# Performance work log

Hardware: AMD Instinct MI355X
Metric: run time of the kernel (lower is better)

The kernel has to match this reference:

```python
import jax, jax.numpy as jnp
import numpy as np

NEG = -1.0e4  # finite stand-in for log(0) of the zero initial state (exp(NEG)==0 in fp32)


def log_g(x):
    # log of g(x) = where(x>=0, x+0.5, sigmoid(x))
    return jnp.where(x >= 0, jnp.log(jax.nn.relu(x) + 0.5), -jax.nn.softplus(-x))


def setup_inputs() -> dict:
    key = jax.random.key(0)
    k1, k2, k3 = jax.random.split(key, 3)
    B, S, D, H, O = 8, 8192, 512, 512, 512
    x = jax.random.normal(k1, (B, S, D), dtype=jnp.float32)
    is_init = jnp.zeros((B,), dtype=bool)  # unused in training mode (h_0 is None)
    W_hg = jax.random.normal(k2, (2 * H, D), dtype=jnp.float32) / np.float32(np.sqrt(D))
    W_out = jax.random.normal(k3, (O, H), dtype=jnp.float32) / np.float32(np.sqrt(H))
    return {"x": x, "is_init": is_init, "W_hg": W_hg, "W_out": W_out}


def reference(x, is_init, W_hg, W_out):
    B, S, _ = x.shape
    H = W_hg.shape[0] // 2
    hg = jnp.einsum('bsd,ed->bse', x, W_hg)          # [B,S,2H]
    hidden, gate = hg[..., :H], hg[..., H:]
    log_coeffs = -jax.nn.softplus(gate)              # log(1 - z)
    log_values = -jax.nn.softplus(-gate) + log_g(hidden)  # log z + log g(h~)
    # prepend h_0 = 0 -> log(h_0) ~ NEG; pad coeffs with a leading 0
    log_values = jnp.concatenate(
        [jnp.full((B, 1, H), NEG, dtype=x.dtype), log_values], axis=1)
    log_coeffs = jnp.pad(log_coeffs, ((0, 0), (1, 0), (0, 0)))
    # Heinsen log-space associative scan
    a_star = jnp.cumsum(log_coeffs, axis=1)
    log_h = a_star + jax.lax.cumlogsumexp(log_values - a_star, axis=1)
    h = jnp.exp(log_h)[:, 1:]                        # drop the h_0 slot -> [B,S,H]
    h_n = h[:, -1:]                                  # [B,1,H]
    out = jnp.einsum('bsh,oh->bso', h, W_out)        # [B,S,O]
    return (out, h_n)
```

## Files before the change

kernel.cpp:

```cpp
#include <hip/hip_runtime.h>
#include <stdint.h>

typedef __bf16 bf16;
typedef bf16 bf16x8 __attribute__((ext_vector_type(8)));
typedef bf16 bf16x4 __attribute__((ext_vector_type(4)));
typedef float f32x4 __attribute__((ext_vector_type(4)));

#define MFMA16(a, b, c) __builtin_amdgcn_mfma_f32_16x16x32_bf16(a, b, c, 0, 0, 0)

__device__ __forceinline__ void gll16(const void* g, void* l) {
    __builtin_amdgcn_global_load_lds(
        (const __attribute__((address_space(1))) void*)g,
        (__attribute__((address_space(3))) void*)l, 16, 0, 0);
}

__device__ __forceinline__ float frcp(float x) { return __builtin_amdgcn_rcpf(x); }

__device__ __forceinline__ float bflo(uint32_t u) {
    union { uint32_t i; float f; } x; x.i = u << 16; return x.f;
}
__device__ __forceinline__ float bfhi(uint32_t u) {
    union { uint32_t i; float f; } x; x.i = u & 0xffff0000u; return x.f;
}
__device__ __forceinline__ uint32_t packcv(float c, float v) {
    union { bf16 b[2]; uint32_t u; } p;
    p.b[0] = (bf16)c; p.b[1] = (bf16)v; return p.u;
}

__global__ __launch_bounds__(256) void conv_kernel(
    const float* __restrict__ X, const float* __restrict__ Whg,
    const float* __restrict__ Wout, bf16* __restrict__ Xbf,
    bf16* __restrict__ Whg_bf, bf16* __restrict__ Wout_bf) {
    int i = blockIdx.x * 256 + threadIdx.x;
    if (i < 8388608) {
        f32x4 v = ((const f32x4*)X)[i];
        ((bf16x4*)Xbf)[i] = __builtin_convertvector(v, bf16x4);
    } else if (i < 8388608 + 131072) {
        int j = i - 8388608;
        f32x4 v = ((const f32x4*)Whg)[j];
        ((bf16x4*)Whg_bf)[j] = __builtin_convertvector(v, bf16x4);
    } else {
        int j = i - (8388608 + 131072);
        f32x4 v = ((const f32x4*)Wout)[j];
        ((bf16x4*)Wout_bf)[j] = __builtin_convertvector(v, bf16x4);
    }
}

__global__ __launch_bounds__(512, 2) void gemm1_kernel(
    const bf16* __restrict__ Xbf, const bf16* __restrict__ W,
    uint32_t* __restrict__ CV) {
    constexpr int K = 512;
    __shared__ bf16 As[2][256 * 64];
    __shared__ bf16 Bh[2][128 * 64];
    __shared__ bf16 Bg[2][128 * 64];

    const int t = threadIdx.x;
    const size_t m0 = (size_t)blockIdx.x * 256;
    const int n0 = blockIdx.y * 128;
    const int w = t >> 6, lane = t & 63;
    const int wm = (w >> 1) * 64, wn = (w & 1) * 64;
    const int r16 = lane & 15, quad = lane >> 4;
    const int sw = r16 & 7;

    f32x4 ah[4][4] = {};
    f32x4 ag[4][4] = {};

    auto stA = [&](int buf, int k0, int rbase) {
        #pragma unroll
        for (int r = rbase; r < rbase + 2; ++r) {
            int g = r * 512 + t; int row = g >> 3; int c8 = (g & 7) ^ (row & 7);
            gll16(Xbf + (m0 + row) * K + k0 + c8 * 8, &As[buf][g * 8]);
        }
    };
    auto stBh = [&](int buf, int k0) {
        #pragma unroll
        for (int r = 0; r < 2; ++r) {
            int g = r * 512 + t; int row = g >> 3; int c8 = (g & 7) ^ (row & 7);
            gll16(W + (size_t)(n0 + row) * K + k0 + c8 * 8, &Bh[buf][g * 8]);
        }
    };
    auto stBg = [&](int buf, int k0) {
        #pragma unroll
        for (int r = 0; r < 2; ++r) {
            int g = r * 512 + t; int row = g >> 3; int c8 = (g & 7) ^ (row & 7);
            gll16(W + (size_t)(512 + n0 + row) * K + k0 + c8 * 8, &Bg[buf][g * 8]);
        }
    };
    auto rdA = [&](bf16x8* d, int buf, int kg) {
        #pragma unroll
        for (int i = 0; i < 4; ++i)
            d[i] = *(const bf16x8*)&As[buf][(wm + i * 16 + r16) * 64 + (kg ^ sw) * 8];
    };
    auto rdBh = [&](bf16x8* d, int buf, int kg) {
        #pragma unroll
        for (int i = 0; i < 4; ++i)
            d[i] = *(const bf16x8*)&Bh[buf][(wn + i * 16 + r16) * 64 + (kg ^ sw) * 8];
    };
    auto rdBg = [&](bf16x8* d, int buf, int kg) {
        #pragma unroll
        for (int i = 0; i < 4; ++i)
            d[i] = *(const bf16x8*)&Bg[buf][(wn + i * 16 + r16) * 64 + (kg ^ sw) * 8];
    };
    auto mmH = [&](const bf16x8* af, const bf16x8* bb) {
        __builtin_amdgcn_s_setprio(1);
        #pragma unroll
        for (int mi = 0; mi < 4; ++mi)
            #pragma unroll
            for (int ni = 0; ni < 4; ++ni)
                ah[mi][ni] = MFMA16(af[mi], bb[ni], ah[mi][ni]);
        __builtin_amdgcn_s_setprio(0);
    };
    auto mmG = [&](const bf16x8* af, const bf16x8* bb) {
        __builtin_amdgcn_s_setprio(1);
        #pragma unroll
        for (int mi = 0; mi < 4; ++mi)
            #pragma unroll
            for (int ni = 0; ni < 4; ++ni)
                ag[mi][ni] = MFMA16(af[mi], bb[ni], ag[mi][ni]);
        __builtin_amdgcn_s_setprio(0);
    };

    stA(0, 0, 0); stA(0, 0, 2); stBh(0, 0); stBg(0, 0);
    stA(1, 64, 0);
    asm volatile("s_waitcnt vmcnt(2)" ::: "memory");
    __builtin_amdgcn_s_barrier();

    #pragma unroll
    for (int tt = 0; tt < 8; ++tt) {
        const int cur = tt & 1, nxt = cur ^ 1;
        const int kn = (tt + 1) * 64;
        bf16x8 af[4], bhf[4], bgf[4];

        rdA(af, cur, quad);
        rdBh(bhf, cur, quad);
        if (tt < 7) stA(nxt, kn, 2);
        if (tt < 7) { asm volatile("s_waitcnt vmcnt(4)" ::: "memory"); }
        else        { asm volatile("s_waitcnt vmcnt(0)" ::: "memory"); }
        __builtin_amdgcn_s_barrier();
        asm volatile("s_waitcnt lgkmcnt(0)" ::: "memory");
        mmH(af, bhf);
        __builtin_amdgcn_s_barrier();

        rdBg(bgf, cur, quad);
        if (tt < 7) stBh(nxt, kn);
        __builtin_amdgcn_s_barrier();
        asm volatile("s_waitcnt lgkmcnt(0)" ::: "memory");
        mmG(af, bgf);
        __builtin_amdgcn_s_barrier();

        rdA(af, cur, 4 + quad);
        rdBh(bhf, cur, 4 + quad);
        if (tt < 7) stBg(nxt, kn);
        __builtin_amdgcn_s_barrier();
        asm volatile("s_waitcnt lgkmcnt(0)" ::: "memory");
        mmH(af, bhf);
        __builtin_amdgcn_s_barrier();

        rdBg(bgf, cur, 4 + quad);
        if (tt < 6) stA(cur, (tt + 2) * 64, 0);
        if (tt < 6)      { asm volatile("s_waitcnt vmcnt(4)" ::: "memory"); }
        else if (tt == 6){ asm volatile("s_waitcnt vmcnt(2)" ::: "memory"); }
        __builtin_amdgcn_s_barrier();
        asm volatile("s_waitcnt lgkmcnt(0)" ::: "memory");
        mmG(af, bgf);
        __builtin_amdgcn_s_barrier();
    }

    #pragma unroll
    for (int mi = 0; mi < 4; ++mi)
        #pragma unroll
        for (int ni = 0; ni < 4; ++ni)
            #pragma unroll
            for (int r = 0; r < 4; ++r) {
                size_t row = m0 + wm + mi * 16 + quad * 4 + r;
                int col = n0 + wn + ni * 16 + r16;
                float hid = ah[mi][ni][r], gat = ag[mi][ni][r];
                float z = frcp(1.f + __expf(-gat));
                float c = 1.f - z;
                float gv = hid >= 0.f ? hid + 0.5f : frcp(1.f + __expf(-hid));
                CV[row * 512 + col] = packcv(c, z * gv);
            }
}

#define NC 64
#define CHUNK 128

__global__ __launch_bounds__(256) void scan1_kernel(
    const uint32_t* __restrict__ CV, float2* __restrict__ agg) {
    int idx = blockIdx.x * 256 + threadIdx.x;
    int h = idx & 511;
    int ch = (idx >> 9) & (NC - 1);
    int b = idx >> 15;
    const uint32_t* p = CV + (((size_t)b * 8192 + (size_t)ch * CHUNK) * 512 + h);
    float C = 1.f, V = 0.f;
    for (int tt = 0; tt < CHUNK; tt += 8) {
        uint32_t u[8];
        #pragma unroll
        for (int j = 0; j < 8; ++j) u[j] = p[(size_t)(tt + j) * 512];
        #pragma unroll
        for (int j = 0; j < 8; ++j) {
            float c = bflo(u[j]), v = bfhi(u[j]);
            C *= c;
            V = c * V + v;
        }
    }
    agg[idx] = make_float2(C, V);
}

__global__ __launch_bounds__(256) void scan2_kernel(
    const float2* __restrict__ agg, float* __restrict__ h0) {
    int idx = blockIdx.x * 256 + threadIdx.x;
    int h = idx & 511;
    int b = idx >> 9;
    float hr = 0.f;
    for (int ch = 0; ch < NC; ++ch) {
        size_t o = ((size_t)b * NC + ch) * 512 + h;
        h0[o] = hr;
        float2 a = agg[o];
        hr = a.x * hr + a.y;
    }
}

__global__ __launch_bounds__(256) void scan3_kernel(
    const uint32_t* __restrict__ CV, const float* __restrict__ h0,
    bf16* __restrict__ Hbf, float* __restrict__ hn) {
    int idx = blockIdx.x * 256 + threadIdx.x;
    int h = idx & 511;
    int ch = (idx >> 9) & (NC - 1);
    int b = idx >> 15;
    size_t base = ((size_t)b * 8192 + (size_t)ch * CHUNK) * 512 + h;
    const uint32_t* p = CV + base;
    bf16* q = Hbf + base;
    float hcur = h0[idx];
    for (int tt = 0; tt < CHUNK; tt += 8) {
        uint32_t u[8];
        #pragma unroll
        for (int j = 0; j < 8; ++j) u[j] = p[(size_t)(tt + j) * 512];
        #pragma unroll
        for (int j = 0; j < 8; ++j) {
            float c = bflo(u[j]), v = bfhi(u[j]);
            hcur = c * hcur + v;
            q[(size_t)(tt + j) * 512] = (bf16)hcur;
        }
    }
    if (ch == NC - 1) hn[b * 512 + h] = hcur;
}

__global__ __launch_bounds__(512, 2) void gemm2_kernel(
    const bf16* __restrict__ Ah, const bf16* __restrict__ Wo,
    float* __restrict__ Out) {
    constexpr int K = 512;
    __shared__ bf16 As[3][256 * 64];
    __shared__ bf16 Bs[3][128 * 64];
    const int t = threadIdx.x;
    const size_t m0 = (size_t)blockIdx.x * 256;
    const int n0 = blockIdx.y * 128;
    const int w = t >> 6, lane = t & 63;
    const int wm = (w >> 1) * 64, wn = (w & 1) * 64;
    const int r16 = lane & 15, quad = lane >> 4;
    const int sw = r16 & 7;
    f32x4 acc[4][4] = {};

    auto stA = [&](int buf, int k0, int r0, int r1) {
        #pragma unroll
        for (int r = r0; r < r1; ++r) {
            int g = r * 512 + t; int row = g >> 3; int c8 = (g & 7) ^ (row & 7);
            gll16(Ah + (m0 + row) * K + k0 + c8 * 8, &As[buf][g * 8]);
        }
    };
    auto stB = [&](int buf, int k0) {
        #pragma unroll
        for (int r = 0; r < 2; ++r) {
            int g = r * 512 + t; int row = g >> 3; int c8 = (g & 7) ^ (row & 7);
            gll16(Wo + (size_t)(n0 + row) * K + k0 + c8 * 8, &Bs[buf][g * 8]);
        }
    };
    auto rdA = [&](bf16x8* d, int buf, int kg) {
        #pragma unroll
        for (int i = 0; i < 4; ++i)
            d[i] = *(const bf16x8*)&As[buf][(wm + i * 16 + r16) * 64 + (kg ^ sw) * 8];
    };
    auto rdB = [&](bf16x8* d, int buf, int kg) {
        #pragma unroll
        for (int i = 0; i < 4; ++i)
            d[i] = *(const bf16x8*)&Bs[buf][(wn + i * 16 + r16) * 64 + (kg ^ sw) * 8];
    };
    auto mm = [&](const bf16x8* af, const bf16x8* bb) {
        __builtin_amdgcn_s_setprio(1);
        #pragma unroll
        for (int mi = 0; mi < 4; ++mi)
            #pragma unroll
            for (int ni = 0; ni < 4; ++ni)
                acc[mi][ni] = MFMA16(af[mi], bb[ni], acc[mi][ni]);
        __builtin_amdgcn_s_setprio(0);
    };

    stA(0, 0, 0, 4); stB(0, 0);
    stA(1, 64, 0, 4); stB(1, 64);
    asm volatile("s_waitcnt vmcnt(6)" ::: "memory");
    __builtin_amdgcn_s_barrier();

    #pragma unroll
    for (int tt = 0; tt < 8; ++tt) {
        const int cur = tt % 3, n2 = (tt + 2) % 3;
        const int k2 = (tt + 2) * 64;
        bf16x8 af[4], bff[4];

        rdA(af, cur, quad);
        rdB(bff, cur, quad);
        if (tt < 6) stA(n2, k2, 0, 3);
        __builtin_amdgcn_s_barrier();
        asm volatile("s_waitcnt lgkmcnt(0)" ::: "memory");
        mm(af, bff);
        __builtin_amdgcn_s_barrier();

        rdA(af, cur, 4 + quad);
        rdB(bff, cur, 4 + quad);
        if (tt < 6) { stA(n2, k2, 3, 4); stB(n2, k2); }
        if (tt < 6)      { asm volatile("s_waitcnt vmcnt(6)" ::: "memory"); }
        else if (tt == 6){ asm volatile("s_waitcnt vmcnt(0)" ::: "memory"); }
        __builtin_amdgcn_s_barrier();
        asm volatile("s_waitcnt lgkmcnt(0)" ::: "memory");
        mm(af, bff);
        __builtin_amdgcn_s_barrier();
    }

    #pragma unroll
    for (int mi = 0; mi < 4; ++mi)
        #pragma unroll
        for (int ni = 0; ni < 4; ++ni)
            #pragma unroll
            for (int r = 0; r < 4; ++r) {
                size_t row = m0 + wm + mi * 16 + quad * 4 + r;
                int col = n0 + wn + ni * 16 + r16;
                Out[row * 512 + col] = acc[mi][ni][r];
            }
}

extern "C" void kernel_launch(void* const* d_in, const int* in_sizes, int n_in,
                              void* d_out, int out_size, void* d_ws, size_t ws_size,
                              hipStream_t stream) {
    const float* x    = (const float*)d_in[0];
    const float* Whg  = (const float*)d_in[2];
    const float* Wout = (const float*)d_in[3];
    float* out = (float*)d_out;

    const int M = 8 * 8192;

    char* ws = (char*)d_ws;
    bf16*     Xbf     = (bf16*)ws;
    bf16*     Hbf     = (bf16*)ws;
    bf16*     Whg_bf  = (bf16*)(ws + 67108864);
    bf16*     Wout_bf = (bf16*)(ws + 68157440);
    uint32_t* CV      = (uint32_t*)(ws + 68681728);
    float2*   agg     = (float2*)(ws + 202899456);
    float*    h0      = (float*)(ws + 204996608);

    conv_kernel<<<33536, 256, 0, stream>>>(x, Whg, Wout, Xbf, Whg_bf, Wout_bf);

    dim3 g1(M / 256, 4);
    gemm1_kernel<<<g1, 512, 0, stream>>>(Xbf, Whg_bf, CV);

    scan1_kernel<<<(8 * NC * 512) / 256, 256, 0, stream>>>(CV, agg);
    scan2_kernel<<<16, 256, 0, stream>>>(agg, h0);
    scan3_kernel<<<(8 * NC * 512) / 256, 256, 0, stream>>>(CV, h0, Hbf,
                                                           out + (size_t)M * 512);

    dim3 g2(M / 256, 4);
    gemm2_kernel<<<g2, 512, 0, stream>>>(Hbf, Wout_bf, out);
}
```

Baseline: 435.2 us.

## Fuse chunk-aggregate scan into GEMM1 epilogue and remap blocks per XCD

Computes the per-chunk (C,V) scan aggregates inside the GEMM1 epilogue, using warp shuffles across quads and an LDS reduction between wave pairs. This removes the separate scan1 pass, which re-read the whole CV buffer from memory. Both GEMMs also switch to a 1D grid whose block index is remapped so that each XCD works on contiguous M rows, aiming for better L2 locality. The cost is extra epilogue work and an LDS barrier in GEMM1.

```diff
diff --git a/kernel.cpp b/kernel.cpp
--- a/kernel.cpp
+++ b/kernel.cpp
@@ -48,15 +48,17 @@
 
 __global__ __launch_bounds__(512, 2) void gemm1_kernel(
     const bf16* __restrict__ Xbf, const bf16* __restrict__ W,
-    uint32_t* __restrict__ CV) {
+    uint32_t* __restrict__ CV, float2* __restrict__ agg) {
     constexpr int K = 512;
     __shared__ bf16 As[2][256 * 64];
     __shared__ bf16 Bh[2][128 * 64];
     __shared__ bf16 Bg[2][128 * 64];
 
     const int t = threadIdx.x;
-    const size_t m0 = (size_t)blockIdx.x * 256;
-    const int n0 = blockIdx.y * 128;
+    const int lin = blockIdx.x;
+    const int xcd = lin & 7, j = lin >> 3;
+    const size_t m0 = (size_t)(xcd * 32 + (j >> 2)) * 256;
+    const int n0 = (j & 3) * 128;
     const int w = t >> 6, lane = t & 63;
     const int wm = (w >> 1) * 64, wn = (w & 1) * 64;
     const int r16 = lane & 15, quad = lane >> 4;
@@ -166,10 +168,14 @@
         __builtin_amdgcn_s_barrier();
     }
 
+    float2* red = (float2*)&As[0][0];
+
     #pragma unroll
-    for (int mi = 0; mi < 4; ++mi)
-        #pragma unroll
-        for (int ni = 0; ni < 4; ++ni)
+    for (int ni = 0; ni < 4; ++ni) {
+        float Cw = 1.f, Vw = 0.f;
+        #pragma unroll
+        for (int mi = 0; mi < 4; ++mi) {
+            float C4 = 1.f, V4 = 0.f;
             #pragma unroll
             for (int r = 0; r < 4; ++r) {
                 size_t row = m0 + wm + mi * 16 + quad * 4 + r;
@@ -178,34 +184,38 @@
                 float z = frcp(1.f + __expf(-gat));
                 float c = 1.f - z;
                 float gv = hid >= 0.f ? hid + 0.5f : frcp(1.f + __expf(-hid));
-                CV[row * 512 + col] = packcv(c, z * gv);
+                float v = z * gv;
+                CV[row * 512 + col] = packcv(c, v);
+                V4 = c * V4 + v;
+                C4 *= c;
             }
+            float Cp = __shfl_xor(C4, 16), Vp = __shfl_xor(V4, 16);
+            float Cn = C4 * Cp;
+            float Vn = (quad & 1) ? (C4 * Vp + V4) : (Cp * V4 + Vp);
+            float Cq = __shfl_xor(Cn, 32), Vq = __shfl_xor(Vn, 32);
+            float C16 = Cn * Cq;
+            float V16 = (quad & 2) ? (Cn * Vq + Vn) : (Cq * Vn + Vq);
+            Vw = C16 * Vw + V16;
+            Cw *= C16;
+        }
+        red[w * 64 + ni * 16 + r16] = make_float2(Cw, Vw);
+    }
+    asm volatile("s_waitcnt lgkmcnt(0)" ::: "memory");
+    __builtin_amdgcn_s_barrier();
+    asm volatile("" ::: "memory");
+    if ((w & 2) == 0) {
+        float2 e = red[w * 64 + lane];
+        float2 l = red[(w + 2) * 64 + lane];
+        int b = (int)(m0 >> 13);
+        int ch = (int)((m0 & 8191) >> 7) + (w >> 2);
+        int col = n0 + (w & 1) * 64 + lane;
+        agg[((size_t)b * 64 + ch) * 512 + col] =
+            make_float2(l.x * e.x, l.x * e.y + l.y);
+    }
 }
 
 #define NC 64
 #define CHUNK 128
-
-__global__ __launch_bounds__(256) void scan1_kernel(
-    const uint32_t* __restrict__ CV, float2* __restrict__ agg) {
-    int idx = blockIdx.x * 256 + threadIdx.x;
-    int h = idx & 511;
-    int ch = (idx >> 9) & (NC - 1);
-    int b = idx >> 15;
-    const uint32_t* p = CV + (((size_t)b * 8192 + (size_t)ch * CHUNK) * 512 + h);
-    float C = 1.f, V = 0.f;
-    for (int tt = 0; tt < CHUNK; tt += 8) {
-        uint32_t u[8];
-        #pragma unroll
-        for (int j = 0; j < 8; ++j) u[j] = p[(size_t)(tt + j) * 512];
-        #pragma unroll
-        for (int j = 0; j < 8; ++j) {
-            float c = bflo(u[j]), v = bfhi(u[j]);
-            C *= c;
-            V = c * V + v;
-        }
-    }
-    agg[idx] = make_float2(C, V);
-}
 
 __global__ __launch_bounds__(256) void scan2_kernel(
     const float2* __restrict__ agg, float* __restrict__ h0) {
@@ -253,8 +263,10 @@
     __shared__ bf16 As[3][256 * 64];
     __shared__ bf16 Bs[3][128 * 64];
     const int t = threadIdx.x;
-    const size_t m0 = (size_t)blockIdx.x * 256;
-    const int n0 = blockIdx.y * 128;
+    const int lin = blockIdx.x;
+    const int xcd = lin & 7, j = lin >> 3;
+    const size_t m0 = (size_t)(xcd * 32 + (j >> 2)) * 256;
+    const int n0 = (j & 3) * 128;
     const int w = t >> 6, lane = t & 63;
     const int wm = (w >> 1) * 64, wn = (w & 1) * 64;
     const int r16 = lane & 15, quad = lane >> 4;
@@ -358,14 +370,11 @@
 
     conv_kernel<<<33536, 256, 0, stream>>>(x, Whg, Wout, Xbf, Whg_bf, Wout_bf);
 
-    dim3 g1(M / 256, 4);
-    gemm1_kernel<<<g1, 512, 0, stream>>>(Xbf, Whg_bf, CV);
-
-    scan1_kernel<<<(8 * NC * 512) / 256, 256, 0, stream>>>(CV, agg);
+    gemm1_kernel<<<1024, 512, 0, stream>>>(Xbf, Whg_bf, CV, agg);
+
     scan2_kernel<<<16, 256, 0, stream>>>(agg, h0);
     scan3_kernel<<<(8 * NC * 512) / 256, 256, 0, stream>>>(CV, h0, Hbf,
                                                            out + (size_t)M * 512);
 
-    dim3 g2(M / 256, 4);
-    gemm2_kernel<<<g2, 512, 0, stream>>>(Hbf, Wout_bf, out);
-}
+    gemm2_kernel<<<1024, 512, 0, stream>>>(Hbf, Wout_bf, out);
+}
```

Result: faster. 400.6 us (-7.9%).
